# Optimization experiments

Measured on AMD Instinct MI355X. Metric: run time of the kernel, lower is better.

## Reference

```python
import jax, jax.numpy as jnp
import numpy as np

N_NODES = 50000
N_EDGES = 800000
NUM_GRAPHS = 4
IN_DIM, HID_DIM, OUT_DIM = 1024, 128, 1
MAX_RISK = 5.0


def gcn_conv(x, W, b, src, dst, n):
    """PyG GCNConv: add self-loops, sym-normalize, gather-GEMM-scatter."""
    loop = jnp.arange(n, dtype=src.dtype)
    s = jnp.concatenate([src, loop])
    d = jnp.concatenate([dst, loop])
    deg = jax.ops.segment_sum(jnp.ones_like(d, dtype=x.dtype), d, num_segments=n)
    dinv = jnp.where(deg > 0, jax.lax.rsqrt(deg), 0.0)
    norm = dinv[s] * dinv[d]  # [E+N]
    xw = x @ W                # dense GEMM first (fewer FLOPs than per-edge)
    msg = xw[s] * norm[:, None]          # irregular gather, [E+N, out]
    out = jax.ops.segment_sum(msg, d, num_segments=n)  # scatter-add
    return out + b


def setup_inputs() -> dict:
    key = jax.random.key(0)
    ks = jax.random.split(key, 12)
    x = jax.random.normal(ks[0], (N_NODES, IN_DIM), dtype=jnp.float32)
    edge_index = jax.random.randint(ks[1], (2, N_EDGES), 0, N_NODES, dtype=jnp.int64)
    batch = jnp.sort(jax.random.randint(ks[2], (N_NODES,), 0, NUM_GRAPHS, dtype=jnp.int64))

    def glorot(k, fan_in, fan_out):
        s = np.sqrt(6.0 / (fan_in + fan_out)).astype(np.float32)
        return jax.random.uniform(k, (fan_in, fan_out), jnp.float32, -s, s)

    params = {
        'W0': glorot(ks[3], IN_DIM, HID_DIM),  'b0': jnp.zeros((HID_DIM,), jnp.float32),
        'W1': glorot(ks[4], HID_DIM, HID_DIM), 'b1': jnp.zeros((HID_DIM,), jnp.float32),
        'W2': glorot(ks[5], HID_DIM, HID_DIM), 'b2': jnp.zeros((HID_DIM,), jnp.float32),
        'Wl1': glorot(ks[6], 2 * HID_DIM, HID_DIM), 'bl1': jnp.zeros((HID_DIM,), jnp.float32),
        'Wl2': glorot(ks[7], HID_DIM, HID_DIM // 2), 'bl2': jnp.zeros((HID_DIM // 2,), jnp.float32),
        'Wl3': glorot(ks[8], HID_DIM // 2, OUT_DIM), 'bl3': jnp.zeros((OUT_DIM,), jnp.float32),
    }
    return dict(x=x, edge_index=edge_index, batch=batch, **params)


def reference(x, edge_index, batch, W0, b0, W1, b1, W2, b2, Wl1, bl1, Wl2, bl2, Wl3, bl3):
    n = x.shape[0]
    src, dst = edge_index[0], edge_index[1]
    h = jax.nn.relu(gcn_conv(x, W0, b0, src, dst, n))
    h = jax.nn.relu(gcn_conv(h, W1, b1, src, dst, n))
    h = jax.nn.relu(gcn_conv(h, W2, b2, src, dst, n))
    # global max pool + global mean pool per graph
    gmax = jax.ops.segment_max(h, batch, num_segments=NUM_GRAPHS)
    gsum = jax.ops.segment_sum(h, batch, num_segments=NUM_GRAPHS)
    cnt = jax.ops.segment_sum(jnp.ones((n,), h.dtype), batch, num_segments=NUM_GRAPHS)
    gmean = gsum / jnp.maximum(cnt, 1.0)[:, None]
    g = jnp.concatenate([gmax, gmean], axis=1)  # [G, 2*hid]
    g = jax.nn.relu(g @ Wl1 + bl1)
    g = jax.nn.relu(g @ Wl2 + bl2)
    out = g @ Wl3 + bl3
    return jnp.minimum(out, MAX_RISK)
```

## Files before the change

kernel.cpp:

```cpp
#include <hip/hip_runtime.h>
#include <math.h>

#define HID 128
#define NGRAPH 4

typedef int idx_t;
typedef float f32x4 __attribute__((ext_vector_type(4)));
typedef _Float16 h8 __attribute__((ext_vector_type(8)));
typedef _Float16 h4 __attribute__((ext_vector_type(4)));

__global__ __launch_bounds__(256) void k_count(const idx_t* __restrict__ dst,
                                               int* __restrict__ cnt, int E) {
  int e = blockIdx.x * 256 + threadIdx.x;
  if (e < E) atomicAdd(&cnt[dst[e]], 1);
}

#define SC 1024
__global__ __launch_bounds__(256) void k_scan1(const int* __restrict__ cnt,
                                               int* __restrict__ bsum, int n) {
  __shared__ int sh[256];
  int base = blockIdx.x * SC + threadIdx.x * 4;
  int s = 0;
#pragma unroll
  for (int j = 0; j < 4; ++j) { int i = base + j; if (i < n) s += cnt[i]; }
  sh[threadIdx.x] = s;
  __syncthreads();
  for (int o = 128; o > 0; o >>= 1) {
    if (threadIdx.x < o) sh[threadIdx.x] += sh[threadIdx.x + o];
    __syncthreads();
  }
  if (threadIdx.x == 0) bsum[blockIdx.x] = sh[0];
}

__global__ __launch_bounds__(64) void k_scan2(const int* __restrict__ bsum,
                                              int* __restrict__ boff,
                                              int* __restrict__ off, int nb, int n) {
  int lane = threadIdx.x;
  int v = (lane < nb) ? bsum[lane] : 0;
  for (int d = 1; d < 64; d <<= 1) {
    int t = __shfl_up(v, d);
    if (lane >= d) v += t;
  }
  int ex = __shfl_up(v, 1);
  if (lane == 0) ex = 0;
  if (lane < nb) boff[lane] = ex;
  if (lane == nb - 1) off[n] = v;
}

__global__ __launch_bounds__(256) void k_scan3(const int* __restrict__ cnt,
                                               const int* __restrict__ boff,
                                               int* __restrict__ off,
                                               float* __restrict__ dinv, int n) {
  __shared__ int sh[256];
  int base = blockIdx.x * SC + threadIdx.x * 4;
  int c[4];
  int s = 0;
#pragma unroll
  for (int j = 0; j < 4; ++j) {
    int i = base + j;
    c[j] = (i < n) ? cnt[i] : 0;
    s += c[j];
  }
  sh[threadIdx.x] = s;
  __syncthreads();
  for (int o = 1; o < 256; o <<= 1) {
    int t = (threadIdx.x >= (unsigned)o) ? sh[threadIdx.x - o] : 0;
    __syncthreads();
    sh[threadIdx.x] += t;
    __syncthreads();
  }
  int ex = sh[threadIdx.x] - s + boff[blockIdx.x];
#pragma unroll
  for (int j = 0; j < 4; ++j) {
    int i = base + j;
    if (i < n) {
      off[i] = ex;
      dinv[i] = 1.0f / sqrtf((float)c[j] + 1.0f);
      ex += c[j];
    }
  }
}

__global__ __launch_bounds__(256) void k_fill(const idx_t* __restrict__ src,
                                              const idx_t* __restrict__ dst,
                                              const int* __restrict__ off,
                                              const float* __restrict__ dinv,
                                              int* __restrict__ fillc,
                                              int2* __restrict__ edata, int E) {
  int e = blockIdx.x * 256 + threadIdx.x;
  if (e < E) {
    int s = src[e], d = dst[e];
    int p = atomicAdd(&fillc[d], 1);
    float w = dinv[s] * dinv[d];
    edata[off[d] + p] = make_int2(s, __float_as_int(w));
  }
}

__global__ __launch_bounds__(256) void k_wsplitf(const float* __restrict__ W,
                                                 _Float16* __restrict__ Wh,
                                                 _Float16* __restrict__ Wl, int K) {
  int i = blockIdx.x * 256 + threadIdx.x;
  if (i >= K * HID) return;
  int j = i & 7, lane = (i >> 3) & 63, ni = (i >> 9) & 7, t = i >> 12;
  int k = t * 32 + (lane >> 4) * 8 + j;
  int col = ni * 16 + (lane & 15);
  float f = W[(size_t)k * HID + col];
  _Float16 h = (_Float16)f;
  Wh[i] = h;
  Wl[i] = (_Float16)(f - (float)h);
}

template <int K, bool F32>
__global__ __launch_bounds__(256, 2) void k_gemm6(const void* __restrict__ Xv,
                                                  const _Float16* __restrict__ Wfh,
                                                  const _Float16* __restrict__ Wfl,
                                                  _Float16* __restrict__ Y16, int M) {
  constexpr int KPW = K / 4;
  constexpr int NT = KPW / 32;
  __shared__ _Float16 AhL[16 * K];
  __shared__ _Float16 AlL[F32 ? 16 * K : 16];
  __shared__ float red[16][132];
  const int tid = threadIdx.x;
  const int wid = tid >> 6, lane = tid & 63;
  const int lrow = lane & 15, kg = lane >> 4;
  const int row0 = blockIdx.x * 16;

  if (F32) {
    const float* X = (const float*)Xv;
#pragma unroll
    for (int r = 0; r < 16; ++r) {
      int grow = row0 + r;
      int grc = (grow < M) ? grow : (M - 1);
      float4 v = *(const float4*)&X[(size_t)grc * K + tid * 4];
      h4 hv, lv;
      float tf[4] = {v.x, v.y, v.z, v.w};
#pragma unroll
      for (int j = 0; j < 4; ++j) {
        _Float16 hh = (_Float16)tf[j];
        hv[j] = hh;
        lv[j] = (_Float16)(tf[j] - (float)hh);
      }
      int swb = (tid * 8) ^ ((r & 7) << 4);
      *(h4*)((char*)AhL + r * (2 * K) + swb) = hv;
      *(h4*)((char*)AlL + r * (2 * K) + swb) = lv;
    }
  } else {
    const _Float16* X = (const _Float16*)Xv;
    int r = (tid * 16) / (2 * K);
    int kb = (tid * 16) % (2 * K);
    int grow = row0 + r;
    int grc = (grow < M) ? grow : (M - 1);
    h8 v = *(const h8*)&X[(size_t)grc * K + kb / 2];
    int swb = kb ^ ((r & 7) << 4);
    *(h8*)((char*)AhL + r * (2 * K) + swb) = v;
  }
  __syncthreads();

  f32x4 acc[8] = {};
#pragma unroll
  for (int t = 0; t < NT; ++t) {
    const int kk = wid * KPW + t * 32;
    h8 ah, al;
    {
      int kb = (kk + kg * 8) * 2;
      int swb = kb ^ ((lrow & 7) << 4);
      ah = *(const h8*)((const char*)AhL + lrow * (2 * K) + swb);
      if (F32) al = *(const h8*)((const char*)AlL + lrow * (2 * K) + swb);
    }
    const size_t fb = (size_t)((wid * NT + t) * 8) * 512 + lane * 8;
#pragma unroll
    for (int ni = 0; ni < 8; ++ni) {
      h8 bh = *(const h8*)(Wfh + fb + ni * 512);
      h8 bl = *(const h8*)(Wfl + fb + ni * 512);
      acc[ni] = __builtin_amdgcn_mfma_f32_16x16x32_f16(ah, bh, acc[ni], 0, 0, 0);
      if (F32)
        acc[ni] = __builtin_amdgcn_mfma_f32_16x16x32_f16(al, bh, acc[ni], 0, 0, 0);
      acc[ni] = __builtin_amdgcn_mfma_f32_16x16x32_f16(ah, bl, acc[ni], 0, 0, 0);
    }
  }

  for (int w = 0; w < 4; ++w) {
    if (wid == w) {
#pragma unroll
      for (int ni = 0; ni < 8; ++ni)
#pragma unroll
        for (int rr = 0; rr < 4; ++rr) {
          int r = kg * 4 + rr, c = ni * 16 + lrow;
          if (w == 0) red[r][c] = acc[ni][rr];
          else red[r][c] += acc[ni][rr];
        }
    }
    __syncthreads();
  }
  int r = tid >> 4, c0 = (tid & 15) * 8;
  int grow = row0 + r;
  if (grow < M) {
    h8 o;
#pragma unroll
    for (int q = 0; q < 8; ++q) o[q] = (_Float16)red[r][c0 + q];
    *(h8*)&Y16[(size_t)grow * HID + c0] = o;
  }
}

__global__ __launch_bounds__(256) void k_agg16(const _Float16* __restrict__ xh,
                                               const float* __restrict__ dinv,
                                               const int* __restrict__ off,
                                               const int2* __restrict__ edata,
                                               const float* __restrict__ bias,
                                               _Float16* __restrict__ hout, int n) {
  int v = blockIdx.x * 4 + (threadIdx.x >> 6);
  if (v >= n) return;
  int lane = threadIdx.x & 63;
  int grp = lane >> 3, gl = lane & 7;
  int fb = gl * 16;
  float acc[16] = {0.f, 0.f, 0.f, 0.f, 0.f, 0.f, 0.f, 0.f,
                   0.f, 0.f, 0.f, 0.f, 0.f, 0.f, 0.f, 0.f};
  int j0 = off[v], j1 = off[v + 1];
  for (int j = j0 + grp; j < j1; j += 8) {
    int2 e = edata[j];
    float w = __int_as_float(e.y);
    h8 m0 = *(const h8*)&xh[(size_t)e.x * HID + fb];
    h8 m1 = *(const h8*)&xh[(size_t)e.x * HID + fb + 8];
#pragma unroll
    for (int q = 0; q < 8; ++q) {
      acc[q] = fmaf(w, (float)m0[q], acc[q]);
      acc[8 + q] = fmaf(w, (float)m1[q], acc[8 + q]);
    }
  }
#pragma unroll
  for (int q = 0; q < 16; ++q) {
    acc[q] += __shfl_xor(acc[q], 8);
    acc[q] += __shfl_xor(acc[q], 16);
    acc[q] += __shfl_xor(acc[q], 32);
  }
  if (grp == 0) {
    float dv = dinv[v], dv2 = dv * dv;
    h8 s0 = *(const h8*)&xh[(size_t)v * HID + fb];
    h8 s1 = *(const h8*)&xh[(size_t)v * HID + fb + 8];
    h8 o0, o1;
#pragma unroll
    for (int q = 0; q < 8; ++q) {
      float a0 = fmaxf(fmaf(dv2, (float)s0[q], acc[q]) + bias[fb + q], 0.f);
      float a1 = fmaxf(fmaf(dv2, (float)s1[q], acc[8 + q]) + bias[fb + 8 + q], 0.f);
      o0[q] = (_Float16)a0;
      o1[q] = (_Float16)a1;
    }
    *(h8*)&hout[(size_t)v * HID + fb] = o0;
    *(h8*)&hout[(size_t)v * HID + fb + 8] = o1;
  }
}

__global__ __launch_bounds__(256) void k_gcnt(const idx_t* __restrict__ batch,
                                              int* __restrict__ gcnt, int n) {
  __shared__ int h[NGRAPH];
  int tid = threadIdx.x;
  if (tid < NGRAPH) h[tid] = 0;
  __syncthreads();
  int i = blockIdx.x * 256 + tid;
  if (i < n) atomicAdd(&h[batch[i]], 1);
  __syncthreads();
  if (tid < NGRAPH && h[tid]) atomicAdd(&gcnt[tid], h[tid]);
}

__global__ __launch_bounds__(128) void k_pool(const _Float16* __restrict__ h,
                                              const idx_t* __restrict__ batch,
                                              float* __restrict__ gmax,
                                              float* __restrict__ gsum, int n) {
  int f = threadIdx.x;
  int v0 = blockIdx.x * 128;
  int cur = -1;
  float mx = 0.f, sm = 0.f;
  for (int i = 0; i < 128; ++i) {
    int v = v0 + i;
    if (v >= n) break;
    int g = batch[v];
    if (g != cur) {
      if (cur >= 0) {
        atomicMax((int*)&gmax[cur * HID + f], __float_as_int(mx));
        atomicAdd(&gsum[cur * HID + f], sm);
      }
      cur = g; mx = 0.f; sm = 0.f;
    }
    float val = (float)h[(size_t)v * HID + f];
    mx = fmaxf(mx, val);
    sm += val;
  }
  if (cur >= 0) {
    atomicMax((int*)&gmax[cur * HID + f], __float_as_int(mx));
    atomicAdd(&gsum[cur * HID + f], sm);
  }
}

__global__ __launch_bounds__(256) void k_mlp(const float* __restrict__ gmax,
                                             const float* __restrict__ gsum,
                                             const int* __restrict__ gcnt,
                                             const float* __restrict__ Wl1,
                                             const float* __restrict__ bl1,
                                             const float* __restrict__ Wl2,
                                             const float* __restrict__ bl2,
                                             const float* __restrict__ Wl3,
                                             const float* __restrict__ bl3,
                                             float* __restrict__ out) {
  __shared__ float G[NGRAPH][2 * HID];
  __shared__ float H1[NGRAPH][HID];
  __shared__ float H2[NGRAPH][HID / 2];
  int t = threadIdx.x;
  for (int i = t; i < NGRAPH * 2 * HID; i += 256) {
    int gi = i >> 8, j = i & 255;
    float val;
    if (j < HID) val = gmax[gi * HID + j];
    else val = gsum[gi * HID + (j - HID)] / fmaxf((float)gcnt[gi], 1.0f);
    G[gi][j] = val;
  }
  __syncthreads();
  for (int i = t; i < NGRAPH * HID; i += 256) {
    int gi = i >> 7, j = i & 127;
    float a = bl1[j];
    for (int k = 0; k < 2 * HID; ++k) a = fmaf(G[gi][k], Wl1[k * HID + j], a);
    H1[gi][j] = fmaxf(a, 0.f);
  }
  __syncthreads();
  {
    int gi = t >> 6, j = t & 63;
    float a = bl2[j];
    for (int k = 0; k < HID; ++k) a = fmaf(H1[gi][k], Wl2[k * 64 + j], a);
    H2[gi][j] = fmaxf(a, 0.f);
  }
  __syncthreads();
  if (t < NGRAPH) {
    float a = bl3[0];
    for (int k = 0; k < 64; ++k) a = fmaf(H2[t][k], Wl3[k], a);
    out[t] = fminf(a, 5.0f);
  }
}

extern "C" void kernel_launch(void* const* d_in, const int* in_sizes, int n_in,
                              void* d_out, int out_size, void* d_ws, size_t ws_size,
                              hipStream_t stream) {
  const float* x   = (const float*)d_in[0];
  const idx_t* ei  = (const idx_t*)d_in[1];
  const idx_t* bat = (const idx_t*)d_in[2];
  const float* W0 = (const float*)d_in[3];  const float* b0 = (const float*)d_in[4];
  const float* W1 = (const float*)d_in[5];  const float* b1 = (const float*)d_in[6];
  const float* W2 = (const float*)d_in[7];  const float* b2 = (const float*)d_in[8];
  const float* Wl1 = (const float*)d_in[9];  const float* bl1 = (const float*)d_in[10];
  const float* Wl2 = (const float*)d_in[11]; const float* bl2 = (const float*)d_in[12];
  const float* Wl3 = (const float*)d_in[13]; const float* bl3 = (const float*)d_in[14];
  float* out = (float*)d_out;

  const int N = in_sizes[2];
  const int E = in_sizes[1] / 2;
  const idx_t* srcv = ei;
  const idx_t* dstv = ei + E;
  const int nb = (N + SC - 1) / SC;

  char* ws = (char*)d_ws;
  size_t o = 0;
  auto alloc = [&](size_t bytes) -> void* {
    void* p = ws + o;
    o = (o + bytes + 255) & ~(size_t)255;
    return p;
  };
  _Float16* xh  = (_Float16*)alloc((size_t)N * HID * 2);
  _Float16* h16 = (_Float16*)alloc((size_t)N * HID * 2);
  float* dinv = (float*)alloc((size_t)N * 4);
  int* cnt    = (int*)alloc((size_t)N * 4);
  int* off    = (int*)alloc((size_t)(N + 1) * 4);
  int* fillc  = (int*)alloc((size_t)N * 4);
  int2* edata = (int2*)alloc((size_t)E * 8);
  int* bsum   = (int*)alloc(64 * 4);
  int* boff   = (int*)alloc(64 * 4);
  _Float16* Wh0 = (_Float16*)alloc((size_t)1024 * HID * 2);
  _Float16* Wl0 = (_Float16*)alloc((size_t)1024 * HID * 2);
  _Float16* Wh1 = (_Float16*)alloc((size_t)HID * HID * 2);
  _Float16* Wlo1 = (_Float16*)alloc((size_t)HID * HID * 2);
  _Float16* Wh2 = (_Float16*)alloc((size_t)HID * HID * 2);
  _Float16* Wlo2 = (_Float16*)alloc((size_t)HID * HID * 2);
  float* gmax = (float*)alloc(NGRAPH * HID * 4);
  float* gsum = (float*)alloc(NGRAPH * HID * 4);
  int* gcnt   = (int*)alloc(NGRAPH * 4);

  hipMemsetAsync(cnt, 0, (size_t)N * 4, stream);
  hipMemsetAsync(fillc, 0, (size_t)N * 4, stream);
  hipMemsetAsync(gmax, 0, NGRAPH * HID * 4, stream);
  hipMemsetAsync(gsum, 0, NGRAPH * HID * 4, stream);
  hipMemsetAsync(gcnt, 0, NGRAPH * 4, stream);

  k_wsplitf<<<(1024 * HID + 255) / 256, 256, 0, stream>>>(W0, Wh0, Wl0, 1024);
  k_wsplitf<<<(HID * HID + 255) / 256, 256, 0, stream>>>(W1, Wh1, Wlo1, HID);
  k_wsplitf<<<(HID * HID + 255) / 256, 256, 0, stream>>>(W2, Wh2, Wlo2, HID);

  k_count<<<(E + 255) / 256, 256, 0, stream>>>(dstv, cnt, E);
  k_scan1<<<nb, 256, 0, stream>>>(cnt, bsum, N);
  k_scan2<<<1, 64, 0, stream>>>(bsum, boff, off, nb, N);
  k_scan3<<<nb, 256, 0, stream>>>(cnt, boff, off, dinv, N);
  k_fill<<<(E + 255) / 256, 256, 0, stream>>>(srcv, dstv, off, dinv, fillc, edata, E);

  const int gblk = (N + 15) / 16;
  const int ablk = (N + 3) / 4;
  k_gemm6<1024, true><<<gblk, 256, 0, stream>>>(x, Wh0, Wl0, xh, N);
  k_agg16<<<ablk, 256, 0, stream>>>(xh, dinv, off, edata, b0, h16, N);
  k_gemm6<HID, false><<<gblk, 256, 0, stream>>>(h16, Wh1, Wlo1, xh, N);
  k_agg16<<<ablk, 256, 0, stream>>>(xh, dinv, off, edata, b1, h16, N);
  k_gemm6<HID, false><<<gblk, 256, 0, stream>>>(h16, Wh2, Wlo2, xh, N);
  k_agg16<<<ablk, 256, 0, stream>>>(xh, dinv, off, edata, b2, h16, N);

  k_gcnt<<<(N + 255) / 256, 256, 0, stream>>>(bat, gcnt, N);
  k_pool<<<(N + 127) / 128, 128, 0, stream>>>(h16, bat, gmax, gsum, N);
  k_mlp<<<1, 256, 0, stream>>>(gmax, gsum, gcnt, Wl1, bl1, Wl2, bl2, Wl3, bl3, out);
}
```

Baseline: 447.5 us.

## Rewrite GEMM with 64-row tiles and double-buffered async global-to-LDS staging

Replaces the 16-row split-K GEMM with a 64-row tile in which each wave owns 16 rows and loops over the whole K. A and the split weight tiles are staged into LDS with double-buffered global_load_lds copies, so the next K slice loads while the current one computes. The fp32 input is now split into high and low fp16 halves after it is read from LDS. Each weight tile is reused across four times as many rows, and the cross-wave LDS reduction is gone. In exchange there is one block barrier per K step, a larger LDS footprint, and per-element 2-byte output stores in place of vectorised ones.

```diff
diff --git a/kernel.cpp b/kernel.cpp
--- a/kernel.cpp
+++ b/kernel.cpp
@@ -7,7 +7,11 @@
 typedef int idx_t;
 typedef float f32x4 __attribute__((ext_vector_type(4)));
 typedef _Float16 h8 __attribute__((ext_vector_type(8)));
-typedef _Float16 h4 __attribute__((ext_vector_type(4)));
+
+#define GLD16(gsrc, ldst)                                                  \
+  __builtin_amdgcn_global_load_lds(                                        \
+      (const __attribute__((address_space(1))) void*)(gsrc),               \
+      (__attribute__((address_space(3))) void*)(ldst), 16, 0, 0)
 
 __global__ __launch_bounds__(256) void k_count(const idx_t* __restrict__ dst,
                                                int* __restrict__ cnt, int E) {
@@ -111,95 +115,96 @@
 }
 
 template <int K, bool F32>
-__global__ __launch_bounds__(256, 2) void k_gemm6(const void* __restrict__ Xv,
-                                                  const _Float16* __restrict__ Wfh,
-                                                  const _Float16* __restrict__ Wfl,
-                                                  _Float16* __restrict__ Y16, int M) {
-  constexpr int KPW = K / 4;
-  constexpr int NT = KPW / 32;
-  __shared__ _Float16 AhL[16 * K];
-  __shared__ _Float16 AlL[F32 ? 16 * K : 16];
-  __shared__ float red[16][132];
+__global__ __launch_bounds__(256) void k_gemm8(const void* __restrict__ Xv,
+                                               const _Float16* __restrict__ Wfh,
+                                               const _Float16* __restrict__ Wfl,
+                                               _Float16* __restrict__ Y16, int M) {
+  constexpr int NT = K / 32;
+  __shared__ __align__(16) char smem[49152];
+  char* Abuf = smem;
+  char* Bhbuf = smem + 16384;
+  char* Blbuf = smem + 32768;
   const int tid = threadIdx.x;
   const int wid = tid >> 6, lane = tid & 63;
   const int lrow = lane & 15, kg = lane >> 4;
-  const int row0 = blockIdx.x * 16;
-
-  if (F32) {
-    const float* X = (const float*)Xv;
-#pragma unroll
-    for (int r = 0; r < 16; ++r) {
-      int grow = row0 + r;
-      int grc = (grow < M) ? grow : (M - 1);
-      float4 v = *(const float4*)&X[(size_t)grc * K + tid * 4];
-      h4 hv, lv;
-      float tf[4] = {v.x, v.y, v.z, v.w};
-#pragma unroll
-      for (int j = 0; j < 4; ++j) {
+  const int row0 = blockIdx.x * 64;
+
+  auto stage = [&](int buf, int t) {
+    const int k0 = t * 32;
+    const char* sBh = (const char*)(Wfh + (size_t)t * 4096);
+    const char* sBl = (const char*)(Wfl + (size_t)t * 4096);
+    char* dBh = Bhbuf + buf * 8192;
+    char* dBl = Blbuf + buf * 8192;
+    GLD16(sBh + tid * 16, dBh + tid * 16);
+    GLD16(sBh + tid * 16 + 4096, dBh + tid * 16 + 4096);
+    GLD16(sBl + tid * 16, dBl + tid * 16);
+    GLD16(sBl + tid * 16 + 4096, dBl + tid * 16 + 4096);
+    char* dA = Abuf + buf * 8192;
+    if (F32) {
+      const float* X = (const float*)Xv;
+#pragma unroll
+      for (int p = 0; p < 2; ++p) {
+        int q = tid * 16 + p * 4096;
+        int r = q >> 7, b = q & 127;
+        int rg = row0 + r; if (rg >= M) rg = M - 1;
+        int bs = b ^ ((r & 7) << 4);
+        GLD16((const char*)&X[(size_t)rg * K + k0] + bs, dA + q);
+      }
+    } else {
+      const _Float16* X = (const _Float16*)Xv;
+      int q = tid * 16;
+      int r = q >> 6, b = q & 63;
+      int rg = row0 + r; if (rg >= M) rg = M - 1;
+      int bs = b ^ ((r & 3) << 4);
+      GLD16((const char*)&X[(size_t)rg * K + k0] + bs, dA + q);
+    }
+  };
+
+  f32x4 acc[8] = {};
+  stage(0, 0);
+  int buf = 0;
+  const int row = wid * 16 + lrow;
+  for (int t = 0; t < NT; ++t) {
+    __syncthreads();
+    if (t + 1 < NT) stage(buf ^ 1, t + 1);
+    h8 ah, al;
+    if (F32) {
+      const char* pA = Abuf + buf * 8192 + row * 128;
+      int sw_ = (row & 7) << 4;
+      f32x4 a0 = *(const f32x4*)(pA + ((kg * 32) ^ sw_));
+      f32x4 a1 = *(const f32x4*)(pA + ((kg * 32 + 16) ^ sw_));
+      float tf[8] = {a0[0], a0[1], a0[2], a0[3], a1[0], a1[1], a1[2], a1[3]};
+#pragma unroll
+      for (int j = 0; j < 8; ++j) {
         _Float16 hh = (_Float16)tf[j];
-        hv[j] = hh;
-        lv[j] = (_Float16)(tf[j] - (float)hh);
+        ah[j] = hh;
+        al[j] = (_Float16)(tf[j] - (float)hh);
       }
-      int swb = (tid * 8) ^ ((r & 7) << 4);
-      *(h4*)((char*)AhL + r * (2 * K) + swb) = hv;
-      *(h4*)((char*)AlL + r * (2 * K) + swb) = lv;
-    }
-  } else {
-    const _Float16* X = (const _Float16*)Xv;
-    int r = (tid * 16) / (2 * K);
-    int kb = (tid * 16) % (2 * K);
-    int grow = row0 + r;
-    int grc = (grow < M) ? grow : (M - 1);
-    h8 v = *(const h8*)&X[(size_t)grc * K + kb / 2];
-    int swb = kb ^ ((r & 7) << 4);
-    *(h8*)((char*)AhL + r * (2 * K) + swb) = v;
-  }
-  __syncthreads();
-
-  f32x4 acc[8] = {};
-#pragma unroll
-  for (int t = 0; t < NT; ++t) {
-    const int kk = wid * KPW + t * 32;
-    h8 ah, al;
-    {
-      int kb = (kk + kg * 8) * 2;
-      int swb = kb ^ ((lrow & 7) << 4);
-      ah = *(const h8*)((const char*)AhL + lrow * (2 * K) + swb);
-      if (F32) al = *(const h8*)((const char*)AlL + lrow * (2 * K) + swb);
-    }
-    const size_t fb = (size_t)((wid * NT + t) * 8) * 512 + lane * 8;
+    } else {
+      const char* pA = Abuf + buf * 8192 + row * 64;
+      ah = *(const h8*)(pA + ((kg * 16) ^ ((row & 3) << 4)));
+    }
+    const char* pBh = Bhbuf + buf * 8192;
+    const char* pBl = Blbuf + buf * 8192;
 #pragma unroll
     for (int ni = 0; ni < 8; ++ni) {
-      h8 bh = *(const h8*)(Wfh + fb + ni * 512);
-      h8 bl = *(const h8*)(Wfl + fb + ni * 512);
+      h8 bh = *(const h8*)(pBh + (ni * 64 + lane) * 16);
+      h8 bl = *(const h8*)(pBl + (ni * 64 + lane) * 16);
       acc[ni] = __builtin_amdgcn_mfma_f32_16x16x32_f16(ah, bh, acc[ni], 0, 0, 0);
       if (F32)
         acc[ni] = __builtin_amdgcn_mfma_f32_16x16x32_f16(al, bh, acc[ni], 0, 0, 0);
       acc[ni] = __builtin_amdgcn_mfma_f32_16x16x32_f16(ah, bl, acc[ni], 0, 0, 0);
     }
-  }
-
-  for (int w = 0; w < 4; ++w) {
-    if (wid == w) {
-#pragma unroll
-      for (int ni = 0; ni < 8; ++ni)
-#pragma unroll
-        for (int rr = 0; rr < 4; ++rr) {
-          int r = kg * 4 + rr, c = ni * 16 + lrow;
-          if (w == 0) red[r][c] = acc[ni][rr];
-          else red[r][c] += acc[ni][rr];
-        }
-    }
-    __syncthreads();
-  }
-  int r = tid >> 4, c0 = (tid & 15) * 8;
-  int grow = row0 + r;
-  if (grow < M) {
-    h8 o;
-#pragma unroll
-    for (int q = 0; q < 8; ++q) o[q] = (_Float16)red[r][c0 + q];
-    *(h8*)&Y16[(size_t)grow * HID + c0] = o;
-  }
+    buf ^= 1;
+  }
+#pragma unroll
+  for (int ni = 0; ni < 8; ++ni)
+#pragma unroll
+    for (int rr = 0; rr < 4; ++rr) {
+      int grow = row0 + wid * 16 + kg * 4 + rr;
+      if (grow < M)
+        Y16[(size_t)grow * HID + ni * 16 + lrow] = (_Float16)acc[ni][rr];
+    }
 }
 
 __global__ __launch_bounds__(256) void k_agg16(const _Float16* __restrict__ xh,
@@ -396,13 +401,13 @@
   k_scan3<<<nb, 256, 0, stream>>>(cnt, boff, off, dinv, N);
   k_fill<<<(E + 255) / 256, 256, 0, stream>>>(srcv, dstv, off, dinv, fillc, edata, E);
 
-  const int gblk = (N + 15) / 16;
+  const int gblk = (N + 63) / 64;
   const int ablk = (N + 3) / 4;
-  k_gemm6<1024, true><<<gblk, 256, 0, stream>>>(x, Wh0, Wl0, xh, N);
+  k_gemm8<1024, true><<<gblk, 256, 0, stream>>>(x, Wh0, Wl0, xh, N);
   k_agg16<<<ablk, 256, 0, stream>>>(xh, dinv, off, edata, b0, h16, N);
-  k_gemm6<HID, false><<<gblk, 256, 0, stream>>>(h16, Wh1, Wlo1, xh, N);
+  k_gemm8<HID, false><<<gblk, 256, 0, stream>>>(h16, Wh1, Wlo1, xh, N);
   k_agg16<<<ablk, 256, 0, stream>>>(xh, dinv, off, edata, b1, h16, N);
-  k_gemm6<HID, false><<<gblk, 256, 0, stream>>>(h16, Wh2, Wlo2, xh, N);
+  k_gemm8<HID, false><<<gblk, 256, 0, stream>>>(h16, Wh2, Wlo2, xh, N);
   k_agg16<<<ablk, 256, 0, stream>>>(xh, dinv, off, edata, b2, h16, N);
 
   k_gcnt<<<(N + 255) / 256, 256, 0, stream>>>(bat, gcnt, N);
```

Result: faster. 369.2 us (-17.5%).
